# Kernel tuning notes

Hardware: AMD Instinct MI355X
Metric: run time of the kernel (lower is better)

Reference implementation:

```python
import jax, jax.numpy as jnp
import numpy as np

N_NODES = 100000
N_EDGES = 1600000
H = 64
TEM = 30.0
LN_EPS = 1e-5


def _mk_params(key):
    ks = jax.random.split(key, 6)
    s = 0.05
    p = {
        # edge_mlp: Linear(2H,H) relu Linear(H,H) relu (act_last=True)
        'We1': jax.random.normal(ks[0], (2 * H, H), jnp.float32) * s,
        'be1': jnp.zeros((H,), jnp.float32),
        'We2': jax.random.normal(ks[1], (H, H), jnp.float32) * s,
        'be2': jnp.zeros((H,), jnp.float32),
        # edge_inf: Linear(H,1)
        'Winf': jax.random.normal(ks[2], (H, 1), jnp.float32) * s,
        'binf': jnp.zeros((1,), jnp.float32),
        # node_mlp: Linear(2H,H) relu Linear(H,H) (no act_last)
        'Wn1': jax.random.normal(ks[3], (2 * H, H), jnp.float32) * s,
        'bn1': jnp.zeros((H,), jnp.float32),
        'Wn2': jax.random.normal(ks[4], (H, H), jnp.float32) * s,
        'bn2': jnp.zeros((H,), jnp.float32),
        # LayerNorm(H)
        'ln_g': jnp.ones((H,), jnp.float32),
        'ln_b': jnp.zeros((H,), jnp.float32),
    }
    return p


def setup_inputs() -> dict:
    key = jax.random.key(0)
    k1, k2, k3, k4 = jax.random.split(key, 4)
    inp = {
        'h': jax.random.normal(k1, (N_NODES, H), jnp.float32),
        'x': jax.random.normal(k2, (N_NODES, 3), jnp.float32),
        'edge_index': jax.random.randint(k3, (2, N_EDGES), 0, N_NODES, jnp.int64),
    }
    inp.update(_mk_params(k4))
    return inp


def _layernorm(z, g, b):
    mu = jnp.mean(z, axis=-1, keepdims=True)
    var = jnp.var(z, axis=-1, keepdims=True)
    return (z - mu) * jax.lax.rsqrt(var + LN_EPS) * g + b


def reference(h, x, edge_index, We1, be1, We2, be2, Winf, binf, Wn1, bn1, Wn2, bn2, ln_g, ln_b):
    src = edge_index[0]
    dst = edge_index[1]
    hi = h[dst]                      # [E, H]
    hj = h[src]                      # [E, H]
    rel_x = x[dst] - x[src]          # [E, 3]
    d_sq = jnp.sum(rel_x ** 2, axis=-1, keepdims=True)  # [E, 1]

    # edge MLP (relu, act_last=True)
    e_in = jnp.concatenate([hi, hj], axis=-1)           # [E, 2H]
    mij = jax.nn.relu(e_in @ We1 + be1)
    mij = jax.nn.relu(mij @ We2 + be2)                  # [E, H]

    eij = mij @ Winf + binf                             # [E, 1]
    edge_dis = jax.nn.sigmoid(TEM / (jnp.sqrt(d_sq) + 1e-8))
    edge_weights = jax.nn.sigmoid(eij * edge_dis)       # [E, 1]

    mi = jax.ops.segment_sum(mij * edge_weights, dst, num_segments=h.shape[0])  # [N, H]

    n_in = jnp.concatenate([mi, h], axis=-1)            # [N, 2H]
    upd = jax.nn.relu(n_in @ Wn1 + bn1) @ Wn2 + bn2     # [N, H] (no act_last)

    h_out = _layernorm(h + upd, ln_g, ln_b)
    return (h_out, x)
```

## Files before the change

### kernel.cpp

```cpp
#include <hip/hip_runtime.h>
#include <hip/hip_bf16.h>
#include <math.h>

#define HDIM 64
#define NN   100000
#define NE   1600000
#define TEMP 30.0f
#define LNEPS 1e-5f

#define GSH   6
#define GSZ   64
#define NB    1563
#define NBLK  64
#define EPB   (NE / NBLK)
#define NCNT  (NB * NBLK)
#define SCANB2 98

typedef __attribute__((ext_vector_type(8))) short bf16x8;
typedef __attribute__((ext_vector_type(4))) float f32x4;

__device__ __forceinline__ short f2bf(float f) {
    __hip_bfloat16 b = __float2bfloat16(f);
    short s; __builtin_memcpy(&s, &b, 2); return s;
}
__device__ __forceinline__ unsigned pk2(float lo, float hi) {
    return (unsigned)(unsigned short)f2bf(lo) | ((unsigned)(unsigned short)f2bf(hi) << 16);
}
__device__ __forceinline__ float bf2f(unsigned u) {
    union { unsigned u; float f; } c; c.u = u << 16; return c.f;
}
__device__ __forceinline__ float sigmoidf_(float z) { return 1.0f / (1.0f + __expf(-z)); }

extern "C" __global__ void __launch_bounds__(256, 2)
front_kernel(const float* __restrict__ h,
             const float* __restrict__ We1, const float* __restrict__ be1,
             unsigned short* __restrict__ Pt, unsigned short* __restrict__ Pb,
             const int* __restrict__ ei, int* __restrict__ cnt3)
{
    __shared__ float fx[4][1024];
    const int b = blockIdx.x;

    if (b < NBLK) {
        int* hbin = (int*)&fx[0][0];
        const int tid = threadIdx.x;
        for (int k = tid; k < NB; k += 256) hbin[k] = 0;
        __syncthreads();
        const int i0 = b * EPB;
        for (int i = i0 + tid; i < i0 + EPB; i += 256)
            atomicAdd(&hbin[ei[NE + i] >> GSH], 1);
        __syncthreads();
        for (int k = tid; k < NB; k += 256)
            cnt3[k * NBLK + b] = hbin[k];
        return;
    }

    const int pb   = b - NBLK;
    const int tid  = threadIdx.x;
    const int wib  = tid >> 6;
    const int lane = tid & 63;
    const int e = lane & 15, g = lane >> 4;
    float* fb = &fx[wib][0];
    const int se = ((e & 1) << 4) | ((e >> 1) & 3);

    bf16x8 At[4][2], Ab[4][2];
    f32x4 b1r[4];
    #pragma unroll
    for (int t = 0; t < 4; ++t) {
        #pragma unroll
        for (int ks = 0; ks < 2; ++ks) {
            bf16x8 a, bb;
            #pragma unroll
            for (int j = 0; j < 8; ++j) {
                a[j]  = f2bf(We1[(32 * ks + 8 * g + j) * 64 + 16 * t + e]);
                bb[j] = f2bf(We1[(64 + 32 * ks + 8 * g + j) * 64 + 16 * t + e]);
            }
            At[t][ks] = a; Ab[t][ks] = bb;
        }
        #pragma unroll
        for (int r = 0; r < 4; ++r) b1r[t][r] = be1[16 * t + 4 * g + r];
    }

    const int gwid = pb * 4 + wib;
    const int nw   = 512 * 4;

    for (int tile = gwid; tile < NN / 16; tile += nw) {
        const int node = tile * 16 + e;

        bf16x8 B[2];
        #pragma unroll
        for (int ks = 0; ks < 2; ++ks) {
            const float4* p = (const float4*)(h + (size_t)node * 64 + ks * 32 + 8 * g);
            const float4 f0 = p[0], f1 = p[1];
            bf16x8 bb;
            bb[0] = f2bf(f0.x); bb[1] = f2bf(f0.y); bb[2] = f2bf(f0.z); bb[3] = f2bf(f0.w);
            bb[4] = f2bf(f1.x); bb[5] = f2bf(f1.y); bb[6] = f2bf(f1.z); bb[7] = f2bf(f1.w);
            B[ks] = bb;
        }

        f32x4 aT[4], aB[4];
        #pragma unroll
        for (int t = 0; t < 4; ++t) {
            aT[t] = b1r[t];
            aB[t] = (f32x4){0.f, 0.f, 0.f, 0.f};
            #pragma unroll
            for (int ks = 0; ks < 2; ++ks) {
                aT[t] = __builtin_amdgcn_mfma_f32_16x16x32_bf16(At[t][ks], B[ks], aT[t], 0, 0, 0);
                aB[t] = __builtin_amdgcn_mfma_f32_16x16x32_bf16(Ab[t][ks], B[ks], aB[t], 0, 0, 0);
            }
        }

        #pragma unroll
        for (int t = 0; t < 4; ++t)
            #pragma unroll
            for (int r = 0; r < 4; ++r)
                fb[e * 64 + ((16 * t + 4 * g + r) ^ se)] = aT[t][r];
        #pragma unroll
        for (int q = 0; q < 2; ++q) {
            const int row = q * 8 + (lane >> 3);
            const int sr  = ((row & 1) << 4) | ((row >> 1) & 3);
            const int c0  = (lane & 7) * 8;
            uint4 o;
            o.x = pk2(fb[row * 64 + ((c0 + 0) ^ sr)], fb[row * 64 + ((c0 + 1) ^ sr)]);
            o.y = pk2(fb[row * 64 + ((c0 + 2) ^ sr)], fb[row * 64 + ((c0 + 3) ^ sr)]);
            o.z = pk2(fb[row * 64 + ((c0 + 4) ^ sr)], fb[row * 64 + ((c0 + 5) ^ sr)]);
            o.w = pk2(fb[row * 64 + ((c0 + 6) ^ sr)], fb[row * 64 + ((c0 + 7) ^ sr)]);
            *(uint4*)((char*)Pt + (size_t)tile * 2048 + q * 1024 + lane * 16) = o;
        }

        #pragma unroll
        for (int t = 0; t < 4; ++t)
            #pragma unroll
            for (int r = 0; r < 4; ++r)
                fb[e * 64 + ((16 * t + 4 * g + r) ^ se)] = aB[t][r];
        #pragma unroll
        for (int q = 0; q < 2; ++q) {
            const int row = q * 8 + (lane >> 3);
            const int sr  = ((row & 1) << 4) | ((row >> 1) & 3);
            const int c0  = (lane & 7) * 8;
            uint4 o;
            o.x = pk2(fb[row * 64 + ((c0 + 0) ^ sr)], fb[row * 64 + ((c0 + 1) ^ sr)]);
            o.y = pk2(fb[row * 64 + ((c0 + 2) ^ sr)], fb[row * 64 + ((c0 + 3) ^ sr)]);
            o.z = pk2(fb[row * 64 + ((c0 + 4) ^ sr)], fb[row * 64 + ((c0 + 5) ^ sr)]);
            o.w = pk2(fb[row * 64 + ((c0 + 6) ^ sr)], fb[row * 64 + ((c0 + 7) ^ sr)]);
            *(uint4*)((char*)Pb + (size_t)tile * 2048 + q * 1024 + lane * 16) = o;
        }
    }
}

extern "C" __global__ void __launch_bounds__(1024)
scanA_kernel(const int* __restrict__ cnt3, int* __restrict__ off3, int* __restrict__ bsum)
{
    __shared__ int sh[1024];
    const int t = threadIdx.x;
    const int i = blockIdx.x * 1024 + t;
    const int v = (i < NCNT) ? cnt3[i] : 0;
    sh[t] = v;
    __syncthreads();
    for (int off = 1; off < 1024; off <<= 1) {
        const int u = (t >= off) ? sh[t - off] : 0;
        __syncthreads();
        sh[t] += u;
        __syncthreads();
    }
    if (i < NCNT) off3[i] = sh[t] - v;
    if (t == 1023) bsum[blockIdx.x] = sh[1023];
}

extern "C" __global__ void __launch_bounds__(128)
scanB_kernel(int* __restrict__ bsum)
{
    __shared__ int sh[128];
    const int t = threadIdx.x;
    const int v = (t < SCANB2) ? bsum[t] : 0;
    sh[t] = v;
    __syncthreads();
    for (int off = 1; off < 128; off <<= 1) {
        const int u = (t >= off) ? sh[t - off] : 0;
        __syncthreads();
        sh[t] += u;
        __syncthreads();
    }
    if (t < SCANB2) bsum[t] = sh[t] - v;
}

extern "C" __global__ void __launch_bounds__(1024)
scanC_kernel(int* __restrict__ off3, const int* __restrict__ bsum)
{
    const int i = blockIdx.x * 1024 + threadIdx.x;
    if (i < NCNT) off3[i] += bsum[blockIdx.x];
}

extern "C" __global__ void __launch_bounds__(256)
scatter3_kernel(const int* __restrict__ ei, const int* __restrict__ off3,
                unsigned* __restrict__ sedge)
{
    __shared__ int cur[NB];
    const int b   = blockIdx.x;
    const int tid = threadIdx.x;
    for (int k = tid; k < NB; k += 256) cur[k] = off3[k * NBLK + b];
    __syncthreads();
    const int i0 = b * EPB;
    for (int i = i0 + tid; i < i0 + EPB; i += 256) {
        const int s = ei[i];
        const int d = ei[NE + i];
        const int pos = atomicAdd(&cur[d >> GSH], 1);
        sedge[pos] = (unsigned)s | ((unsigned)(d & (GSZ - 1)) << 17);
    }
}

extern "C" __global__ void __launch_bounds__(256)
sort2_kernel(const unsigned* __restrict__ sedge, const int* __restrict__ off3,
             int2* __restrict__ spair)
{
    __shared__ int hist[GSZ], base[GSZ], curs[GSZ];
    const int tid = threadIdx.x;
    const int b   = blockIdx.x;
    const int r0  = off3[b * NBLK];
    const int r1  = (b == NB - 1) ? NE : off3[(b + 1) * NBLK];

    if (tid < GSZ) hist[tid] = 0;
    __syncthreads();
    for (int i = r0 + tid; i < r1; i += 256)
        atomicAdd(&hist[(sedge[i] >> 17) & (GSZ - 1)], 1);
    __syncthreads();
    if (tid == 0) {
        int run = 0;
        for (int j = 0; j < GSZ; ++j) { base[j] = run; run += hist[j]; }
    }
    __syncthreads();
    if (tid < GSZ) curs[tid] = base[tid];
    __syncthreads();
    for (int i = r0 + tid; i < r1; i += 256) {
        const unsigned pk = sedge[i];
        const int dl = (pk >> 17) & (GSZ - 1);
        const int pos = r0 + atomicAdd(&curs[dl], 1);
        spair[pos] = make_int2((int)(pk & 0x1FFFFu), (b << GSH) | dl);
    }
}

extern "C" __global__ void __launch_bounds__(256, 2)
edge_kernel_sorted(const unsigned short* __restrict__ Pt, const unsigned short* __restrict__ Pb,
                   const float* __restrict__ x, const int2* __restrict__ spair,
                   const float* __restrict__ We2, const float* __restrict__ be2,
                   const float* __restrict__ Winf, const float* __restrict__ binf,
                   float* __restrict__ mi)
{
    __shared__ float fx[4][1024];
    const int tid  = threadIdx.x;
    const int wib  = tid >> 6;
    const int lane = tid & 63;
    const int e = lane & 15, g = lane >> 4;
    float* fb = &fx[wib][0];
    const int se = ((e & 1) << 4) | ((e >> 1) & 3);

    bf16x8 A2[4][2];
    f32x4 b2r[4], wir[4];
    #pragma unroll
    for (int t = 0; t < 4; ++t) {
        #pragma unroll
        for (int ks = 0; ks < 2; ++ks) {
            bf16x8 a;
            #pragma unroll
            for (int j = 0; j < 8; ++j)
                a[j] = f2bf(We2[(32 * ks + 8 * g + j) * 64 + 16 * t + e]);
            A2[t][ks] = a;
        }
        #pragma unroll
        for (int r = 0; r < 4; ++r) {
            b2r[t][r] = be2[16 * t + 4 * g + r];
            wir[t][r] = Winf[16 * t + 4 * g + r];
        }
    }
    const float binf0 = binf[0];

    const int NT     = NE / 16;
    const int nwaves = gridDim.x * 4;
    const int gwid   = blockIdx.x * 4 + wib;
    const int chunk  = (NT + nwaves - 1) / nwaves;
    const int t0 = gwid * chunk;
    const int t1 = (t0 + chunk < NT) ? t0 + chunk : NT;

    float racc  = 0.f;
    int   rrow  = -1;

    for (int tile = t0; tile < t1; ++tile) {
        const int eid = tile * 16 + e;
        const int2 sd = spair[eid];
        const int sN = sd.x;
        const int dN = sd.y;

        const float dx = x[dN * 3 + 0] - x[sN * 3 + 0];
        const float dy = x[dN * 3 + 1] - x[sN * 3 + 1];
        const float dz = x[dN * 3 + 2] - x[sN * 3 + 2];
        const float dsq = dx * dx + dy * dy + dz * dz;
        const float edis = sigmoidf_(TEMP / (sqrtf(dsq) + 1e-8f));

        bf16x8 B2[2];
        #pragma unroll
        for (int ks = 0; ks < 2; ++ks) {
            const uint4 ut = *(const uint4*)(Pt + (size_t)dN * 64 + 32 * ks + 8 * g);
            const uint4 ub = *(const uint4*)(Pb + (size_t)sN * 64 + 32 * ks + 8 * g);
            bf16x8 bb;
            unsigned tw, bw;
            tw = ut.x; bw = ub.x;
            bb[0] = f2bf(fmaxf(bf2f(tw & 0xffffu) + bf2f(bw & 0xffffu), 0.f));
            bb[1] = f2bf(fmaxf(bf2f(tw >> 16)     + bf2f(bw >> 16),     0.f));
            tw = ut.y; bw = ub.y;
            bb[2] = f2bf(fmaxf(bf2f(tw & 0xffffu) + bf2f(bw & 0xffffu), 0.f));
            bb[3] = f2bf(fmaxf(bf2f(tw >> 16)     + bf2f(bw >> 16),     0.f));
            tw = ut.z; bw = ub.z;
            bb[4] = f2bf(fmaxf(bf2f(tw & 0xffffu) + bf2f(bw & 0xffffu), 0.f));
            bb[5] = f2bf(fmaxf(bf2f(tw >> 16)     + bf2f(bw >> 16),     0.f));
            tw = ut.w; bw = ub.w;
            bb[6] = f2bf(fmaxf(bf2f(tw & 0xffffu) + bf2f(bw & 0xffffu), 0.f));
            bb[7] = f2bf(fmaxf(bf2f(tw >> 16)     + bf2f(bw >> 16),     0.f));
            B2[ks] = bb;
        }

        f32x4 acc2[4];
        #pragma unroll
        for (int t = 0; t < 4; ++t) {
            acc2[t] = b2r[t];
            #pragma unroll
            for (int ks = 0; ks < 2; ++ks)
                acc2[t] = __builtin_amdgcn_mfma_f32_16x16x32_bf16(A2[t][ks], B2[ks], acc2[t], 0, 0, 0);
        }

        float m[4][4];
        float p = 0.f;
        #pragma unroll
        for (int t = 0; t < 4; ++t)
            #pragma unroll
            for (int r = 0; r < 4; ++r) {
                m[t][r] = fmaxf(acc2[t][r], 0.f);
                p = fmaf(m[t][r], wir[t][r], p);
            }
        p += __shfl_xor(p, 16);
        p += __shfl_xor(p, 32);
        const float w = sigmoidf_((p + binf0) * edis);

        #pragma unroll
        for (int t = 0; t < 4; ++t)
            #pragma unroll
            for (int r = 0; r < 4; ++r)
                fb[e * 64 + ((16 * t + 4 * g + r) ^ se)] = m[t][r] * w;

        #pragma unroll
        for (int i = 0; i < 16; ++i) {
            const int row = __builtin_amdgcn_readlane(dN, i);
            const int si = ((i & 1) << 4) | ((i >> 1) & 3);
            const float v = fb[i * 64 + (lane ^ si)];
            if (row != rrow) {
                if (rrow >= 0) atomicAdd(mi + (size_t)rrow * 64 + lane, racc);
                rrow = row; racc = v;
            } else {
                racc += v;
            }
        }
    }
    if (rrow >= 0) atomicAdd(mi + (size_t)rrow * 64 + lane, racc);
}

extern "C" __global__ void __launch_bounds__(256, 2)
edge_kernel_unsorted(const unsigned short* __restrict__ Pt, const unsigned short* __restrict__ Pb,
                     const float* __restrict__ x, const int* __restrict__ ei,
                     const float* __restrict__ We2, const float* __restrict__ be2,
                     const float* __restrict__ Winf, const float* __restrict__ binf,
                     float* __restrict__ mi)
{
    __shared__ float fx[4][1024];
    const int tid  = threadIdx.x;
    const int wib  = tid >> 6;
    const int lane = tid & 63;
    const int e = lane & 15, g = lane >> 4;
    float* fb = &fx[wib][0];
    const int se = ((e & 1) << 4) | ((e >> 1) & 3);

    bf16x8 A2[4][2];
    f32x4 b2r[4], wir[4];
    #pragma unroll
    for (int t = 0; t < 4; ++t) {
        #pragma unroll
        for (int ks = 0; ks < 2; ++ks) {
            bf16x8 a;
            #pragma unroll
            for (int j = 0; j < 8; ++j)
                a[j] = f2bf(We2[(32 * ks + 8 * g + j) * 64 + 16 * t + e]);
            A2[t][ks] = a;
        }
        #pragma unroll
        for (int r = 0; r < 4; ++r) {
            b2r[t][r] = be2[16 * t + 4 * g + r];
            wir[t][r] = Winf[16 * t + 4 * g + r];
        }
    }
    const float binf0 = binf[0];

    const int gwid = blockIdx.x * 4 + wib;
    const int nw   = gridDim.x * 4;

    for (int tile = gwid; tile < NE / 16; tile += nw) {
        const int eid = tile * 16 + e;
        const int sN = ei[eid];
        const int dN = ei[NE + eid];

        const float dx = x[dN * 3 + 0] - x[sN * 3 + 0];
        const float dy = x[dN * 3 + 1] - x[sN * 3 + 1];
        const float dz = x[dN * 3 + 2] - x[sN * 3 + 2];
        const float dsq = dx * dx + dy * dy + dz * dz;
        const float edis = sigmoidf_(TEMP / (sqrtf(dsq) + 1e-8f));

        bf16x8 B2[2];
        #pragma unroll
        for (int ks = 0; ks < 2; ++ks) {
            const uint4 ut = *(const uint4*)(Pt + (size_t)dN * 64 + 32 * ks + 8 * g);
            const uint4 ub = *(const uint4*)(Pb + (size_t)sN * 64 + 32 * ks + 8 * g);
            bf16x8 bb;
            unsigned tw, bw;
            tw = ut.x; bw = ub.x;
            bb[0] = f2bf(fmaxf(bf2f(tw & 0xffffu) + bf2f(bw & 0xffffu), 0.f));
            bb[1] = f2bf(fmaxf(bf2f(tw >> 16)     + bf2f(bw >> 16),     0.f));
            tw = ut.y; bw = ub.y;
            bb[2] = f2bf(fmaxf(bf2f(tw & 0xffffu) + bf2f(bw & 0xffffu), 0.f));
            bb[3] = f2bf(fmaxf(bf2f(tw >> 16)     + bf2f(bw >> 16),     0.f));
            tw = ut.z; bw = ub.z;
            bb[4] = f2bf(fmaxf(bf2f(tw & 0xffffu) + bf2f(bw & 0xffffu), 0.f));
            bb[5] = f2bf(fmaxf(bf2f(tw >> 16)     + bf2f(bw >> 16),     0.f));
            tw = ut.w; bw = ub.w;
            bb[6] = f2bf(fmaxf(bf2f(tw & 0xffffu) + bf2f(bw & 0xffffu), 0.f));
            bb[7] = f2bf(fmaxf(bf2f(tw >> 16)     + bf2f(bw >> 16),     0.f));
            B2[ks] = bb;
        }

        f32x4 acc2[4];
        #pragma unroll
        for (int t = 0; t < 4; ++t) {
            acc2[t] = b2r[t];
            #pragma unroll
            for (int ks = 0; ks < 2; ++ks)
                acc2[t] = __builtin_amdgcn_mfma_f32_16x16x32_bf16(A2[t][ks], B2[ks], acc2[t], 0, 0, 0);
        }

        float m[4][4];
        float p = 0.f;
        #pragma unroll
        for (int t = 0; t < 4; ++t)
            #pragma unroll
            for (int r = 0; r < 4; ++r) {
                m[t][r] = fmaxf(acc2[t][r], 0.f);
                p = fmaf(m[t][r], wir[t][r], p);
            }
        p += __shfl_xor(p, 16);
        p += __shfl_xor(p, 32);
        const float w = sigmoidf_((p + binf0) * edis);

        #pragma unroll
        for (int t = 0; t < 4; ++t)
            #pragma unroll
            for (int r = 0; r < 4; ++r)
                fb[e * 64 + ((16 * t + 4 * g + r) ^ se)] = m[t][r] * w;

        #pragma unroll
        for (int i = 0; i < 16; ++i) {
            const int row = __shfl(dN, i);
            const int si = ((i & 1) << 4) | ((i >> 1) & 3);
            const float v = fb[i * 64 + (lane ^ si)];
            atomicAdd(mi + (size_t)row * 64 + lane, v);
        }
    }
}

extern "C" __global__ void __launch_bounds__(256, 2)
node_kernel(const float* __restrict__ h, const float* __restrict__ mi_,
            const float* __restrict__ Wn1, const float* __restrict__ bn1,
            const float* __restrict__ Wn2, const float* __restrict__ bn2,
            const float* __restrict__ lng, const float* __restrict__ lnb,
            float* __restrict__ out)
{
    __shared__ unsigned xlds[4][16 * 32];
    const int tid  = threadIdx.x;
    const int wib  = tid >> 6;
    const int lane = tid & 63;
    const int e = lane & 15, g = lane >> 4;
    unsigned* tb = &xlds[wib][0];
    const int sw = (e & 7) << 2;

    bf16x8 A1[4][4], A2[4][2];
    f32x4 b1r[4], b2r[4], gr[4], br[4];
    #pragma unroll
    for (int t = 0; t < 4; ++t) {
        #pragma unroll
        for (int ks = 0; ks < 4; ++ks) {
            bf16x8 a;
            #pragma unroll
            for (int j = 0; j < 8; ++j)
                a[j] = f2bf(Wn1[(32 * ks + 8 * g + j) * 64 + 16 * t + e]);
            A1[t][ks] = a;
        }
        #pragma unroll
        for (int ks = 0; ks < 2; ++ks) {
            bf16x8 a;
            #pragma unroll
            for (int j = 0; j < 8; ++j)
                a[j] = f2bf(Wn2[(32 * ks + 8 * g + j) * 64 + 16 * t + e]);
            A2[t][ks] = a;
        }
        #pragma unroll
        for (int r = 0; r < 4; ++r) {
            b1r[t][r] = bn1[16 * t + 4 * g + r];
            b2r[t][r] = bn2[16 * t + 4 * g + r];
            gr[t][r]  = lng[16 * t + 4 * g + r];
            br[t][r]  = lnb[16 * t + 4 * g + r];
        }
    }

    const int gwid = blockIdx.x * 4 + wib;
    const int nw   = gridDim.x * 4;

    for (int tile = gwid; tile < NN / 16; tile += nw) {
        const int node = tile * 16 + e;

        bf16x8 B1[4];
        #pragma unroll
        for (int ks = 0; ks < 4; ++ks) {
            const float* srcp = (ks < 2) ? mi_ : h;
            const float4* p = (const float4*)(srcp + (size_t)node * 64 + (ks & 1) * 32 + 8 * g);
            const float4 f0 = p[0], f1 = p[1];
            bf16x8 b;
            b[0] = f2bf(f0.x); b[1] = f2bf(f0.y); b[2] = f2bf(f0.z); b[3] = f2bf(f0.w);
            b[4] = f2bf(f1.x); b[5] = f2bf(f1.y); b[6] = f2bf(f1.z); b[7] = f2bf(f1.w);
            B1[ks] = b;
        }

        f32x4 acc1[4];
        #pragma unroll
        for (int t = 0; t < 4; ++t) {
            acc1[t] = b1r[t];
            #pragma unroll
            for (int ks = 0; ks < 4; ++ks)
                acc1[t] = __builtin_amdgcn_mfma_f32_16x16x32_bf16(A1[t][ks], B1[ks], acc1[t], 0, 0, 0);
        }

        #pragma unroll
        for (int t = 0; t < 4; ++t) {
            const float r0 = fmaxf(acc1[t][0], 0.f), r1 = fmaxf(acc1[t][1], 0.f);
            const float r2 = fmaxf(acc1[t][2], 0.f), r3 = fmaxf(acc1[t][3], 0.f);
            tb[e * 32 + ((8 * t + 2 * g + 0) ^ sw)] = pk2(r0, r1);
            tb[e * 32 + ((8 * t + 2 * g + 1) ^ sw)] = pk2(r2, r3);
        }
        bf16x8 B2[2];
        #pragma unroll
        for (int ks = 0; ks < 2; ++ks) {
            union { uint4 u; bf16x8 b; } cvt;
            cvt.u = *(const uint4*)&tb[e * 32 + ((16 * ks + 4 * g) ^ sw)];
            B2[ks] = cvt.b;
        }

        f32x4 acc2[4];
        #pragma unroll
        for (int t = 0; t < 4; ++t) {
            acc2[t] = b2r[t];
            #pragma unroll
            for (int ks = 0; ks < 2; ++ks)
                acc2[t] = __builtin_amdgcn_mfma_f32_16x16x32_bf16(A2[t][ks], B2[ks], acc2[t], 0, 0, 0);
        }

        float z[4][4];
        float s1 = 0.f, s2 = 0.f;
        #pragma unroll
        for (int t = 0; t < 4; ++t) {
            const float4 hres = *(const float4*)(h + (size_t)node * 64 + 16 * t + 4 * g);
            #pragma unroll
            for (int r = 0; r < 4; ++r) {
                z[t][r] = acc2[t][r] + hres[r];
                s1 += z[t][r];
                s2 = fmaf(z[t][r], z[t][r], s2);
            }
        }
        s1 += __shfl_xor(s1, 16); s1 += __shfl_xor(s1, 32);
        s2 += __shfl_xor(s2, 16); s2 += __shfl_xor(s2, 32);
        const float mu   = s1 * (1.0f / 64.0f);
        const float var  = s2 * (1.0f / 64.0f) - mu * mu;
        const float rstd = rsqrtf(var + LNEPS);

        #pragma unroll
        for (int t = 0; t < 4; ++t) {
            float4 o;
            #pragma unroll
            for (int r = 0; r < 4; ++r)
                o[r] = (z[t][r] - mu) * rstd * gr[t][r] + br[t][r];
            *(float4*)(out + (size_t)node * 64 + 16 * t + 4 * g) = o;
        }
    }
}

extern "C" void kernel_launch(void* const* d_in, const int* in_sizes, int n_in,
                              void* d_out, int out_size, void* d_ws, size_t ws_size,
                              hipStream_t stream)
{
    const float* h    = (const float*)d_in[0];
    const float* x    = (const float*)d_in[1];
    const int*   ei   = (const int*)d_in[2];
    const float* We1  = (const float*)d_in[3];
    const float* be1  = (const float*)d_in[4];
    const float* We2  = (const float*)d_in[5];
    const float* be2  = (const float*)d_in[6];
    const float* Winf = (const float*)d_in[7];
    const float* binf = (const float*)d_in[8];
    const float* Wn1  = (const float*)d_in[9];
    const float* bn1  = (const float*)d_in[10];
    const float* Wn2  = (const float*)d_in[11];
    const float* bn2  = (const float*)d_in[12];
    const float* lng  = (const float*)d_in[13];
    const float* lnb  = (const float*)d_in[14];
    float* out = (float*)d_out;

    const size_t mi_bytes = (size_t)NN * HDIM * sizeof(float);
    const size_t p_bytes  = (size_t)NN * HDIM * sizeof(unsigned short);
    const size_t sp_bytes = (size_t)NE * sizeof(int2);
    const size_t se_bytes = (size_t)NE * sizeof(unsigned);
    const size_t c3_bytes = (size_t)NCNT * sizeof(int);

    const size_t need_sorted = mi_bytes + 2 * p_bytes + sp_bytes;

    if (ws_size >= need_sorted &&
        mi_bytes >= se_bytes + 2 * c3_bytes + SCANB2 * sizeof(int)) {
        char* ws = (char*)d_ws;
        float*          mi    = (float*)ws;              ws += mi_bytes;
        unsigned short* Pt    = (unsigned short*)ws;     ws += p_bytes;
        unsigned short* Pb    = (unsigned short*)ws;     ws += p_bytes;
        int2*           spair = (int2*)ws;

        char* mis = (char*)mi;
        unsigned* sedge = (unsigned*)mis;
        int*      cnt3  = (int*)(mis + se_bytes);
        int*      off3  = (int*)(mis + se_bytes + c3_bytes);
        int*      bsum  = (int*)(mis + se_bytes + 2 * c3_bytes);

        hipMemcpyAsync(out + (size_t)NN * HDIM, x, (size_t)NN * 3 * sizeof(float),
                       hipMemcpyDeviceToDevice, stream);

        front_kernel<<<NBLK + 512, 256, 0, stream>>>(h, We1, be1, Pt, Pb, ei, cnt3);
        scanA_kernel<<<SCANB2, 1024, 0, stream>>>(cnt3, off3, bsum);
        scanB_kernel<<<1, 128, 0, stream>>>(bsum);
        scanC_kernel<<<SCANB2, 1024, 0, stream>>>(off3, bsum);
        scatter3_kernel<<<NBLK, 256, 0, stream>>>(ei, off3, sedge);
        sort2_kernel<<<NB, 256, 0, stream>>>(sedge, off3, spair);
        hipMemsetAsync(mi, 0, mi_bytes, stream);
        edge_kernel_sorted<<<2048, 256, 0, stream>>>(Pt, Pb, x, spair, We2, be2, Winf, binf, mi);
        node_kernel<<<512, 256, 0, stream>>>(h, mi, Wn1, bn1, Wn2, bn2, lng, lnb, out);
    } else {
        float* mi;
        unsigned short* Pt;
        unsigned short* Pb;
        if (ws_size >= mi_bytes + 2 * p_bytes) {
            mi = (float*)d_ws;
            Pt = (unsigned short*)((char*)d_ws + mi_bytes);
            Pb = (unsigned short*)((char*)d_ws + mi_bytes + p_bytes);
        } else {
            mi = out;
            Pt = (unsigned short*)d_ws;
            Pb = (unsigned short*)((char*)d_ws + p_bytes);
        }

        hipMemsetAsync(mi, 0, mi_bytes, stream);
        hipMemcpyAsync(out + (size_t)NN * HDIM, x, (size_t)NN * 3 * sizeof(float),
                       hipMemcpyDeviceToDevice, stream);

        front_kernel<<<NBLK + 512, 256, 0, stream>>>(h, We1, be1, Pt, Pb, ei,
                                                     (int*)((char*)d_ws));
        edge_kernel_unsorted<<<2048, 256, 0, stream>>>(Pt, Pb, x, ei, We2, be2, Winf, binf, mi);
        node_kernel<<<512, 256, 0, stream>>>(h, mi, Wn1, bn1, Wn2, bn2, lng, lnb, out);
    }
}
```

Before: 220.6 us.

## Switch edge projections to fp16 with packed add-relu, vectorize LDS stores

The precomputed per-node projections Pt/Pb and the second edge-layer weights are now stored as fp16 instead of bf16. The edge kernels combine them with packed half-precision add plus a bitmask ReLU rather than unpacking each element to fp32, and use the f16 MFMA. The edge kernel's shared-memory write of weighted messages is changed from scalar stores to float4 stores, with lane-dependent permutation to keep the swizzle. The scatter kernel is launched with 1024 threads per block instead of 256. This cuts ALU work in the gather loop, but fp16 range and precision could differ from bf16 for large projection values.

```diff
diff --git a/kernel.cpp b/kernel.cpp
--- a/kernel.cpp
+++ b/kernel.cpp
@@ -1,5 +1,6 @@
 #include <hip/hip_runtime.h>
 #include <hip/hip_bf16.h>
+#include <hip/hip_fp16.h>
 #include <math.h>
 
 #define HDIM 64
@@ -18,6 +19,7 @@
 
 typedef __attribute__((ext_vector_type(8))) short bf16x8;
 typedef __attribute__((ext_vector_type(4))) float f32x4;
+typedef _Float16 __attribute__((ext_vector_type(2))) h2t;
 
 __device__ __forceinline__ short f2bf(float f) {
     __hip_bfloat16 b = __float2bfloat16(f);
@@ -26,8 +28,20 @@
 __device__ __forceinline__ unsigned pk2(float lo, float hi) {
     return (unsigned)(unsigned short)f2bf(lo) | ((unsigned)(unsigned short)f2bf(hi) << 16);
 }
-__device__ __forceinline__ float bf2f(unsigned u) {
-    union { unsigned u; float f; } c; c.u = u << 16; return c.f;
+__device__ __forceinline__ short f2h(float f) {
+    __half h = __float2half(f);
+    short s; __builtin_memcpy(&s, &h, 2); return s;
+}
+__device__ __forceinline__ unsigned pk2h(float lo, float hi) {
+    return (unsigned)(unsigned short)f2h(lo) | ((unsigned)(unsigned short)f2h(hi) << 16);
+}
+__device__ __forceinline__ unsigned pk_add_relu(unsigned a, unsigned b) {
+    h2t x, y;
+    __builtin_memcpy(&x, &a, 4); __builtin_memcpy(&y, &b, 4);
+    h2t r = x + y;
+    unsigned u; __builtin_memcpy(&u, &r, 4);
+    const unsigned msk = ((u & 0x80008000u) >> 15) * 0xFFFFu;
+    return u & ~msk;
 }
 __device__ __forceinline__ float sigmoidf_(float z) { return 1.0f / (1.0f + __expf(-z)); }
 
@@ -120,10 +134,10 @@
             const int sr  = ((row & 1) << 4) | ((row >> 1) & 3);
             const int c0  = (lane & 7) * 8;
             uint4 o;
-            o.x = pk2(fb[row * 64 + ((c0 + 0) ^ sr)], fb[row * 64 + ((c0 + 1) ^ sr)]);
-            o.y = pk2(fb[row * 64 + ((c0 + 2) ^ sr)], fb[row * 64 + ((c0 + 3) ^ sr)]);
-            o.z = pk2(fb[row * 64 + ((c0 + 4) ^ sr)], fb[row * 64 + ((c0 + 5) ^ sr)]);
-            o.w = pk2(fb[row * 64 + ((c0 + 6) ^ sr)], fb[row * 64 + ((c0 + 7) ^ sr)]);
+            o.x = pk2h(fb[row * 64 + ((c0 + 0) ^ sr)], fb[row * 64 + ((c0 + 1) ^ sr)]);
+            o.y = pk2h(fb[row * 64 + ((c0 + 2) ^ sr)], fb[row * 64 + ((c0 + 3) ^ sr)]);
+            o.z = pk2h(fb[row * 64 + ((c0 + 4) ^ sr)], fb[row * 64 + ((c0 + 5) ^ sr)]);
+            o.w = pk2h(fb[row * 64 + ((c0 + 6) ^ sr)], fb[row * 64 + ((c0 + 7) ^ sr)]);
             *(uint4*)((char*)Pt + (size_t)tile * 2048 + q * 1024 + lane * 16) = o;
         }
 
@@ -138,10 +152,10 @@
             const int sr  = ((row & 1) << 4) | ((row >> 1) & 3);
             const int c0  = (lane & 7) * 8;
             uint4 o;
-            o.x = pk2(fb[row * 64 + ((c0 + 0) ^ sr)], fb[row * 64 + ((c0 + 1) ^ sr)]);
-            o.y = pk2(fb[row * 64 + ((c0 + 2) ^ sr)], fb[row * 64 + ((c0 + 3) ^ sr)]);
-            o.z = pk2(fb[row * 64 + ((c0 + 4) ^ sr)], fb[row * 64 + ((c0 + 5) ^ sr)]);
-            o.w = pk2(fb[row * 64 + ((c0 + 6) ^ sr)], fb[row * 64 + ((c0 + 7) ^ sr)]);
+            o.x = pk2h(fb[row * 64 + ((c0 + 0) ^ sr)], fb[row * 64 + ((c0 + 1) ^ sr)]);
+            o.y = pk2h(fb[row * 64 + ((c0 + 2) ^ sr)], fb[row * 64 + ((c0 + 3) ^ sr)]);
+            o.z = pk2h(fb[row * 64 + ((c0 + 4) ^ sr)], fb[row * 64 + ((c0 + 5) ^ sr)]);
+            o.w = pk2h(fb[row * 64 + ((c0 + 6) ^ sr)], fb[row * 64 + ((c0 + 7) ^ sr)]);
             *(uint4*)((char*)Pb + (size_t)tile * 2048 + q * 1024 + lane * 16) = o;
         }
     }
@@ -190,17 +204,17 @@
     if (i < NCNT) off3[i] += bsum[blockIdx.x];
 }
 
-extern "C" __global__ void __launch_bounds__(256)
+extern "C" __global__ void __launch_bounds__(1024)
 scatter3_kernel(const int* __restrict__ ei, const int* __restrict__ off3,
                 unsigned* __restrict__ sedge)
 {
     __shared__ int cur[NB];
     const int b   = blockIdx.x;
     const int tid = threadIdx.x;
-    for (int k = tid; k < NB; k += 256) cur[k] = off3[k * NBLK + b];
+    for (int k = tid; k < NB; k += 1024) cur[k] = off3[k * NBLK + b];
     __syncthreads();
     const int i0 = b * EPB;
-    for (int i = i0 + tid; i < i0 + EPB; i += 256) {
+    for (int i = i0 + tid; i < i0 + EPB; i += 1024) {
         const int s = ei[i];
         const int d = ei[NE + i];
         const int pos = atomicAdd(&cur[d >> GSH], 1);
@@ -251,7 +265,8 @@
     const int lane = tid & 63;
     const int e = lane & 15, g = lane >> 4;
     float* fb = &fx[wib][0];
-    const int se = ((e & 1) << 4) | ((e >> 1) & 3);
+    const int s2  = (e >> 1) & 3;
+    const int b16 = (e & 1) << 4;
 
     bf16x8 A2[4][2];
     f32x4 b2r[4], wir[4];
@@ -262,7 +277,7 @@
             bf16x8 a;
             #pragma unroll
             for (int j = 0; j < 8; ++j)
-                a[j] = f2bf(We2[(32 * ks + 8 * g + j) * 64 + 16 * t + e]);
+                a[j] = f2h(We2[(32 * ks + 8 * g + j) * 64 + 16 * t + e]);
             A2[t][ks] = a;
         }
         #pragma unroll
@@ -300,21 +315,12 @@
         for (int ks = 0; ks < 2; ++ks) {
             const uint4 ut = *(const uint4*)(Pt + (size_t)dN * 64 + 32 * ks + 8 * g);
             const uint4 ub = *(const uint4*)(Pb + (size_t)sN * 64 + 32 * ks + 8 * g);
-            bf16x8 bb;
-            unsigned tw, bw;
-            tw = ut.x; bw = ub.x;
-            bb[0] = f2bf(fmaxf(bf2f(tw & 0xffffu) + bf2f(bw & 0xffffu), 0.f));
-            bb[1] = f2bf(fmaxf(bf2f(tw >> 16)     + bf2f(bw >> 16),     0.f));
-            tw = ut.y; bw = ub.y;
-            bb[2] = f2bf(fmaxf(bf2f(tw & 0xffffu) + bf2f(bw & 0xffffu), 0.f));
-            bb[3] = f2bf(fmaxf(bf2f(tw >> 16)     + bf2f(bw >> 16),     0.f));
-            tw = ut.z; bw = ub.z;
-            bb[4] = f2bf(fmaxf(bf2f(tw & 0xffffu) + bf2f(bw & 0xffffu), 0.f));
-            bb[5] = f2bf(fmaxf(bf2f(tw >> 16)     + bf2f(bw >> 16),     0.f));
-            tw = ut.w; bw = ub.w;
-            bb[6] = f2bf(fmaxf(bf2f(tw & 0xffffu) + bf2f(bw & 0xffffu), 0.f));
-            bb[7] = f2bf(fmaxf(bf2f(tw >> 16)     + bf2f(bw >> 16),     0.f));
-            B2[ks] = bb;
+            union { uint4 u; bf16x8 b; } cvt;
+            cvt.u.x = pk_add_relu(ut.x, ub.x);
+            cvt.u.y = pk_add_relu(ut.y, ub.y);
+            cvt.u.z = pk_add_relu(ut.z, ub.z);
+            cvt.u.w = pk_add_relu(ut.w, ub.w);
+            B2[ks] = cvt.b;
         }
 
         f32x4 acc2[4];
@@ -323,7 +329,7 @@
             acc2[t] = b2r[t];
             #pragma unroll
             for (int ks = 0; ks < 2; ++ks)
-                acc2[t] = __builtin_amdgcn_mfma_f32_16x16x32_bf16(A2[t][ks], B2[ks], acc2[t], 0, 0, 0);
+                acc2[t] = __builtin_amdgcn_mfma_f32_16x16x32_f16(A2[t][ks], B2[ks], acc2[t], 0, 0, 0);
         }
 
         float m[4][4];
@@ -340,10 +346,17 @@
         const float w = sigmoidf_((p + binf0) * edis);
 
         #pragma unroll
-        for (int t = 0; t < 4; ++t)
-            #pragma unroll
-            for (int r = 0; r < 4; ++r)
-                fb[e * 64 + ((16 * t + 4 * g + r) ^ se)] = m[t][r] * w;
+        for (int t = 0; t < 4; ++t) {
+            const float a0 = m[t][0] * w, a1 = m[t][1] * w;
+            const float a2 = m[t][2] * w, a3 = m[t][3] * w;
+            const bool sA = (s2 & 1), sB = (s2 & 2);
+            const float u0 = sA ? a1 : a0, u1 = sA ? a0 : a1;
+            const float u2 = sA ? a3 : a2, u3 = sA ? a2 : a3;
+            float4 v;
+            v.x = sB ? u2 : u0; v.y = sB ? u3 : u1;
+            v.z = sB ? u0 : u2; v.w = sB ? u1 : u3;
+            *(float4*)&fb[e * 64 + ((16 * t + 4 * g) ^ b16)] = v;
+        }
 
         #pragma unroll
         for (int i = 0; i < 16; ++i) {
@@ -385,7 +398,7 @@
             bf16x8 a;
             #pragma unroll
             for (int j = 0; j < 8; ++j)
-                a[j] = f2bf(We2[(32 * ks + 8 * g + j) * 64 + 16 * t + e]);
+                a[j] = f2h(We2[(32 * ks + 8 * g + j) * 64 + 16 * t + e]);
             A2[t][ks] = a;
         }
         #pragma unroll
@@ -415,21 +428,12 @@
         for (int ks = 0; ks < 2; ++ks) {
             const uint4 ut = *(const uint4*)(Pt + (size_t)dN * 64 + 32 * ks + 8 * g);
             const uint4 ub = *(const uint4*)(Pb + (size_t)sN * 64 + 32 * ks + 8 * g);
-            bf16x8 bb;
-            unsigned tw, bw;
-            tw = ut.x; bw = ub.x;
-            bb[0] = f2bf(fmaxf(bf2f(tw & 0xffffu) + bf2f(bw & 0xffffu), 0.f));
-            bb[1] = f2bf(fmaxf(bf2f(tw >> 16)     + bf2f(bw >> 16),     0.f));
-            tw = ut.y; bw = ub.y;
-            bb[2] = f2bf(fmaxf(bf2f(tw & 0xffffu) + bf2f(bw & 0xffffu), 0.f));
-            bb[3] = f2bf(fmaxf(bf2f(tw >> 16)     + bf2f(bw >> 16),     0.f));
-            tw = ut.z; bw = ub.z;
-            bb[4] = f2bf(fmaxf(bf2f(tw & 0xffffu) + bf2f(bw & 0xffffu), 0.f));
-            bb[5] = f2bf(fmaxf(bf2f(tw >> 16)     + bf2f(bw >> 16),     0.f));
-            tw = ut.w; bw = ub.w;
-            bb[6] = f2bf(fmaxf(bf2f(tw & 0xffffu) + bf2f(bw & 0xffffu), 0.f));
-            bb[7] = f2bf(fmaxf(bf2f(tw >> 16)     + bf2f(bw >> 16),     0.f));
-            B2[ks] = bb;
+            union { uint4 u; bf16x8 b; } cvt;
+            cvt.u.x = pk_add_relu(ut.x, ub.x);
+            cvt.u.y = pk_add_relu(ut.y, ub.y);
+            cvt.u.z = pk_add_relu(ut.z, ub.z);
+            cvt.u.w = pk_add_relu(ut.w, ub.w);
+            B2[ks] = cvt.b;
         }
 
         f32x4 acc2[4];
@@ -438,7 +442,7 @@
             acc2[t] = b2r[t];
             #pragma unroll
             for (int ks = 0; ks < 2; ++ks)
-                acc2[t] = __builtin_amdgcn_mfma_f32_16x16x32_bf16(A2[t][ks], B2[ks], acc2[t], 0, 0, 0);
+                acc2[t] = __builtin_amdgcn_mfma_f32_16x16x32_f16(A2[t][ks], B2[ks], acc2[t], 0, 0, 0);
         }
 
         float m[4][4];
@@ -644,7 +648,7 @@
         scanA_kernel<<<SCANB2, 1024, 0, stream>>>(cnt3, off3, bsum);
         scanB_kernel<<<1, 128, 0, stream>>>(bsum);
         scanC_kernel<<<SCANB2, 1024, 0, stream>>>(off3, bsum);
-        scatter3_kernel<<<NBLK, 256, 0, stream>>>(ei, off3, sedge);
+        scatter3_kernel<<<NBLK, 1024, 0, stream>>>(ei, off3, sedge);
         sort2_kernel<<<NB, 256, 0, stream>>>(sedge, off3, spair);
         hipMemsetAsync(mi, 0, mi_bytes, stream);
         edge_kernel_sorted<<<2048, 256, 0, stream>>>(Pt, Pb, x, spair, We2, be2, Winf, binf, mi);
```

New measurement: 196.6 us. -10.8%, faster.
